# Performance work log

Measured on AMD Instinct MI355X. Metric: run time of the kernel, lower is better.

The kernel has to match this reference:

```python
import jax, jax.numpy as jnp
import numpy as np

GRID = (32, 32)          # 448 // 14
IMG = (448, 448)
SIGMA = 4.0              # anomalib AnomalyMapGenerator default smoothing


def _l2norm(x, axis=-1, eps=1e-12):
    return x / jnp.clip(jnp.linalg.norm(x, axis=axis, keepdims=True), eps, None)


def _gaussian_blur(x, sigma=SIGMA):
    # kornia-style: kernel_size = 2*int(4*sigma+0.5)+1, reflect padding, separable conv
    radius = int(4.0 * sigma + 0.5)
    t = jnp.arange(-radius, radius + 1, dtype=x.dtype)
    k = jnp.exp(-0.5 * (t / sigma) ** 2)
    k = k / k.sum()
    xp = jnp.pad(x, ((0, 0), (0, 0), (radius, radius), (radius, radius)), mode='reflect')
    kh = k.reshape(1, 1, -1, 1)
    kw = k.reshape(1, 1, 1, -1)
    dn = ('NCHW', 'OIHW', 'NCHW')
    y = jax.lax.conv_general_dilated(xp, kh, (1, 1), 'VALID', dimension_numbers=dn)
    return jax.lax.conv_general_dilated(y, kw, (1, 1), 'VALID', dimension_numbers=dn)


def setup_inputs() -> dict:
    key = jax.random.key(0)
    k1, k2 = jax.random.split(key)
    features = jax.random.normal(k1, (8, 1024, 384), dtype=jnp.float32)
    memory_bank = jax.random.normal(k2, (65536, 384), dtype=jnp.float32)
    return {"features": features, "memory_bank": memory_bank}


def reference(features, memory_bank):
    # features: (B, N, D) patch tokens from DINOv2; memory_bank: (M, D)
    b, n, _ = features.shape
    f = _l2norm(features)                 # F.normalize(features, p=2, dim=1) on flattened patches
    mb = _l2norm(memory_bank)             # bank stores normalized embeddings
    sim = jnp.einsum('bnd,md->bnm', f, mb)            # (B, N, M) cosine similarity
    dists = jnp.clip(1.0 - sim, 0.0, 2.0)
    min_dists = dists.min(axis=2)                     # k = num_neighbours = 1 -> row min
    num_top = max(int(n * 0.01), 1)
    top_vals = jax.lax.top_k(min_dists, num_top)[0]
    pred_score = top_vals.mean(axis=1, keepdims=True) # (B, 1)
    amap = min_dists.reshape(b, 1, *GRID)
    amap = jax.image.resize(amap, (b, 1, *IMG), method='bilinear')
    anomaly_map = _gaussian_blur(amap)                # (B, 1, H, W)
    return pred_score, anomaly_map
```

## Files before the change

kernel.cpp:

```cpp
#include <hip/hip_runtime.h>
#include <hip/hip_bf16.h>

#define NROW_F 8192
#define NROW_B 65536
#define KDIM   384
#define BM 128
#define BN 128
#define NSUB 16
#define NGRP (NROW_B / (BN * NSUB))
#define NBM  (NROW_F / BM)
#define NWG  (NBM * NGRP)

#define LDSA 0
#define LDSB 49152
#define LDSS 73728
#define LDSR 49152
#define LDS_TOT 81920

typedef int   i32x4 __attribute__((ext_vector_type(4)));
typedef float f32x4 __attribute__((ext_vector_type(4)));

static __device__ __forceinline__ void stage16(const void* g, void* l) {
  __builtin_amdgcn_global_load_lds(
      (const __attribute__((address_space(1))) unsigned int*)g,
      (__attribute__((address_space(3))) unsigned int*)l, 16, 0, 0);
}

__global__ __launch_bounds__(256) void quantize_rows_kernel(
    const float* __restrict__ in, char* __restrict__ out8,
    float* __restrict__ scales, int nrows) {
  int row  = blockIdx.x * 4 + (threadIdx.x >> 6);
  int lane = threadIdx.x & 63;
  if (row >= nrows) return;
  const float* r = in + (size_t)row * KDIM;
  float v[6];
  float ss = 0.f, mx = 0.f;
#pragma unroll
  for (int i = 0; i < 6; ++i) {
    v[i] = r[lane + i * 64];
    ss += v[i] * v[i];
    mx = fmaxf(mx, fabsf(v[i]));
  }
#pragma unroll
  for (int d = 1; d < 64; d <<= 1) {
    ss += __shfl_xor(ss, d, 64);
    mx = fmaxf(mx, __shfl_xor(mx, d, 64));
  }
  mx = fmaxf(mx, 1e-30f);
  float inv = rsqrtf(fmaxf(ss, 1e-24f));
  float scl = 127.0f / mx;
  if (lane == 0) scales[row] = mx * inv * (1.0f / 127.0f);
  char* o = out8 + (size_t)row * KDIM;
#pragma unroll
  for (int i = 0; i < 6; ++i)
    o[lane + i * 64] = (char)__float2int_rn(v[i] * scl);
}

__global__ __launch_bounds__(256, 2) void maxsim_kernel(
    const char* __restrict__ F8,
    const char* __restrict__ B8,
    const float* __restrict__ sA,
    const float* __restrict__ sB,
    float* __restrict__ partial) {
  __shared__ __align__(16) char smem[LDS_TOT];

  const int tid  = threadIdx.x;
  const int wv   = tid >> 6;
  const int lane = tid & 63;
  const int l15  = lane & 15;
  const int lhi  = lane >> 4;
  const int wr   = wv >> 1;
  const int wc   = wv & 1;

  const int wg  = (blockIdx.x & 7) * (NWG / 8) + (blockIdx.x >> 3);
  const int bm  = wg & (NBM - 1);
  const int grp = wg >> 6;
  const size_t brow = (size_t)bm * BM;

  const int srow = tid >> 2;
  const int gsw  = (tid & 3) ^ ((tid >> 3) & 3);

  {
    const char* gA = F8 + (size_t)(brow + srow) * KDIM + gsw * 16;
    char* lA = smem + LDSA + wv * 1024;
#pragma unroll
    for (int kt = 0; kt < 6; ++kt) {
      stage16(gA + kt * 64,             lA + kt * 8192);
      stage16(gA + kt * 64 + 64 * KDIM, lA + kt * 8192 + 4096);
    }
  }
  {
    const char* gs = (const char*)(sB + (size_t)grp * 2048) + tid * 16;
    stage16(gs,        smem + LDSS + wv * 1024);
    stage16(gs + 4096, smem + LDSS + 4096 + wv * 1024);
  }

  auto stageB = [&](int s2, int koff, int buf) {
    const char* g = B8 + ((size_t)grp * 2048 + s2 * 128 + srow) * KDIM
                    + koff * 64 + gsw * 16;
    char* l = smem + LDSB + buf * 8192 + wv * 1024;
    stage16(g, l);
    stage16(g + (size_t)64 * KDIM, l + 4096);
  };
  stageB(0, 0, 0);
  stageB(0, 1, 1);
  stageB(0, 2, 2);

  const int cof = ((l15 >> 1) & 3) << 4;

  auto ldA8 = [&](int k6, int m) -> i32x4 {
    int byte = k6 * 8192 + (wr * 64 + m * 16 + l15) * 64 + ((lhi << 4) ^ cof);
    return *reinterpret_cast<const i32x4*>(smem + LDSA + byte);
  };
  auto ldB8 = [&](int buf, int n) -> i32x4 {
    int byte = buf * 8192 + (wc * 64 + n * 16 + l15) * 64 + ((lhi << 4) ^ cof);
    return *reinterpret_cast<const i32x4*>(smem + LDSB + byte);
  };

  i32x4 acc[4][4];
  f32x4 vm[4];
#pragma unroll
  for (int m = 0; m < 4; ++m) {
    vm[m] = f32x4{-1e30f, -1e30f, -1e30f, -1e30f};
#pragma unroll
    for (int n = 0; n < 4; ++n) acc[m][n] = i32x4{0, 0, 0, 0};
  }

  asm volatile("s_waitcnt vmcnt(4)" ::: "memory");
  __builtin_amdgcn_s_barrier();

  i32x4 a[6][4];
#pragma unroll
  for (int k6 = 0; k6 < 6; ++k6)
#pragma unroll
    for (int m = 0; m < 4; ++m) a[k6][m] = ldA8(k6, m);

  i32x4 bA[4], bB[4];
#pragma unroll
  for (int n = 0; n < 4; ++n) bA[n] = ldB8(0, n);
  asm volatile("s_waitcnt lgkmcnt(0)" ::: "memory");

#define PHASE(K6, BC, BN_) do {                                               \
    asm volatile("s_waitcnt vmcnt(2)" ::: "memory");   \
    __builtin_amdgcn_s_barrier();                      \
    __builtin_amdgcn_sched_barrier(0);                                        \
    _Pragma("unroll")                                                         \
    for (int n = 0; n < 4; ++n) BN_[n] = ldB8(((K6) + 1) % 3, n);             \
    {                                                                         \
      const int s2 = ((K6) < 3) ? sub : ((sub + 1) & (NSUB - 1));             \
      stageB(s2, ((K6) + 3) % 6, (K6) % 3);                                   \
    }                                                                         \
    __builtin_amdgcn_sched_barrier(0);                                        \
    __builtin_amdgcn_s_setprio(1);                                            \
    _Pragma("unroll")                                                         \
    for (int n = 0; n < 4; ++n)                                               \
      _Pragma("unroll")                                                       \
      for (int m = 0; m < 4; ++m)                                             \
        acc[m][n] = __builtin_amdgcn_mfma_i32_16x16x64_i8(                    \
            a[K6][m], BC[n], acc[m][n], 0, 0, 0);                             \
    __builtin_amdgcn_s_setprio(0);                                            \
    asm volatile("s_waitcnt lgkmcnt(0)" ::: "memory");                        \
    __builtin_amdgcn_sched_barrier(0);                                        \
  } while (0)

  for (int sub = 0; sub < NSUB; ++sub) {
    PHASE(0, bA, bB);
    PHASE(1, bB, bA);
    PHASE(2, bA, bB);
    PHASE(3, bB, bA);
    PHASE(4, bA, bB);
    PHASE(5, bB, bA);
    float sb[4];
#pragma unroll
    for (int n = 0; n < 4; ++n)
      sb[n] = *reinterpret_cast<const float*>(
          smem + LDSS + (sub * 128 + wc * 64 + n * 16 + l15) * 4);
#pragma unroll
    for (int m = 0; m < 4; ++m) {
#pragma unroll
      for (int n = 0; n < 4; ++n)
#pragma unroll
        for (int j = 0; j < 4; ++j)
          vm[m][j] = fmaxf(vm[m][j], (float)acc[m][n][j] * sb[n]);
#pragma unroll
      for (int n = 0; n < 4; ++n) acc[m][n] = i32x4{0, 0, 0, 0};
    }
  }
#undef PHASE

  asm volatile("s_waitcnt vmcnt(0)" ::: "memory");
#pragma unroll
  for (int d = 1; d < 16; d <<= 1)
#pragma unroll
    for (int m = 0; m < 4; ++m)
#pragma unroll
      for (int j = 0; j < 4; ++j)
        vm[m][j] = fmaxf(vm[m][j], __shfl_xor(vm[m][j], d, 64));

  float* red = (float*)(smem + LDSR);
  __syncthreads();
  if (l15 == 0) {
#pragma unroll
    for (int m = 0; m < 4; ++m)
#pragma unroll
      for (int j = 0; j < 4; ++j)
        red[wc * 128 + wr * 64 + m * 16 + lhi * 4 + j] = vm[m][j];
  }
  __syncthreads();
  if (tid < BM) {
    float x = fmaxf(red[tid], red[128 + tid]);
    partial[(size_t)grp * NROW_F + brow + tid] = x * sA[brow + tid];
  }
}

__global__ __launch_bounds__(256) void combine_kernel(
    const float* __restrict__ partial, float* __restrict__ md) {
  int r = blockIdx.x * 256 + threadIdx.x;
  if (r >= NROW_F) return;
  float m = -1e30f;
#pragma unroll
  for (int c = 0; c < NGRP; ++c) m = fmaxf(m, partial[(size_t)c * NROW_F + r]);
  float d = 1.0f - m;
  d = fminf(fmaxf(d, 0.0f), 2.0f);
  md[r] = d;
}

__global__ __launch_bounds__(256) void topk_kernel(
    const float* __restrict__ md, float* __restrict__ out) {
  __shared__ float buf[1024];
  __shared__ float svals[256];
  __shared__ int   sidx[256];
  int b = blockIdx.x, tid = threadIdx.x;
  for (int i = tid; i < 1024; i += 256) buf[i] = md[b * 1024 + i];
  __syncthreads();
  float total = 0.f;
  for (int it = 0; it < 10; ++it) {
    float best = -1e30f; int bi = 0;
    for (int i = tid; i < 1024; i += 256)
      if (buf[i] > best) { best = buf[i]; bi = i; }
    svals[tid] = best; sidx[tid] = bi;
    __syncthreads();
    for (int s = 128; s > 0; s >>= 1) {
      if (tid < s && svals[tid + s] > svals[tid]) {
        svals[tid] = svals[tid + s]; sidx[tid] = sidx[tid + s];
      }
      __syncthreads();
    }
    if (tid == 0) { total += svals[0]; buf[sidx[0]] = -1e30f; }
    __syncthreads();
  }
  if (tid == 0) out[b] = total * 0.1f;
}

__global__ __launch_bounds__(256) void build_w_kernel(float* __restrict__ W) {
  int idx = blockIdx.x * 256 + threadIdx.x;
  if (idx >= 448 * 32) return;
  int y = idx >> 5, g = idx & 31;
  float ksum = 0.f, acc = 0.f;
#pragma unroll
  for (int t = -16; t <= 16; ++t) {
    float ft = (float)t * 0.25f;
    float kv = expf(-0.5f * ft * ft);
    ksum += kv;
    int p = y + t;
    p = (p < 0) ? -p : ((p > 447) ? 894 - p : p);
    float src = ((float)p + 0.5f) * (1.0f / 14.0f) - 0.5f;
    float fl = floorf(src);
    int i0 = (int)fl;
    float fr = src - fl;
    int c0 = i0 < 0 ? 0 : (i0 > 31 ? 31 : i0);
    int i1 = i0 + 1;
    int c1 = i1 < 0 ? 0 : (i1 > 31 ? 31 : i1);
    float w = 0.f;
    if (c0 == g) w += 1.0f - fr;
    if (c1 == g) w += fr;
    acc += kv * w;
  }
  W[idx] = acc / ksum;
}

__global__ __launch_bounds__(256) void map_stage1_kernel(
    const float* __restrict__ md, const float* __restrict__ W,
    float* __restrict__ tmp) {
  int idx = blockIdx.x * 256 + threadIdx.x;
  if (idx >= 8 * 448 * 32) return;
  int gx = idx & 31;
  int y  = (idx >> 5) % 448;
  int b  = idx / (448 * 32);
  const float* w = W + y * 32;
  const float* m = md + b * 1024 + gx;
  float s = 0.f;
#pragma unroll
  for (int gy = 0; gy < 32; ++gy) s += w[gy] * m[gy * 32];
  tmp[idx] = s;
}

__global__ __launch_bounds__(256) void map_stage2_kernel(
    const float* __restrict__ tmp, const float* __restrict__ W,
    float* __restrict__ out) {
  int idx = blockIdx.x * 256 + threadIdx.x;
  if (idx >= 8 * 448 * 448) return;
  int x    = idx % 448;
  int ypos = idx / 448;
  const float* w = W + x * 32;
  const float* t = tmp + ypos * 32;
  float s = 0.f;
#pragma unroll
  for (int gx = 0; gx < 32; ++gx) s += w[gx] * t[gx];
  out[idx] = s;
}

extern "C" void kernel_launch(void* const* d_in, const int* in_sizes, int n_in,
                              void* d_out, int out_size, void* d_ws, size_t ws_size,
                              hipStream_t stream) {
  const float* features = (const float*)d_in[0];
  const float* bank     = (const float*)d_in[1];
  float* out = (float*)d_out;

  char* ws = (char*)d_ws;
  char*  mb8     = ws;
  char*  f8      = ws + 25165824;
  float* sB      = (float*)(ws + 28311552);
  float* sA      = (float*)(ws + 28573696);
  float* partial = (float*)(ws + 28606464);
  float* md      = (float*)(ws + 29655040);
  float* W       = (float*)(ws + 29687808);
  float* tmp     = (float*)(ws + 29745152);

  quantize_rows_kernel<<<NROW_B / 4, 256, 0, stream>>>(bank, mb8, sB, NROW_B);
  quantize_rows_kernel<<<NROW_F / 4, 256, 0, stream>>>(features, f8, sA, NROW_F);
  maxsim_kernel<<<NWG, 256, 0, stream>>>(f8, mb8, sA, sB, partial);
  combine_kernel<<<NROW_F / 256, 256, 0, stream>>>(partial, md);
  topk_kernel<<<8, 256, 0, stream>>>(md, out);
  build_w_kernel<<<(448 * 32 + 255) / 256, 256, 0, stream>>>(W);
  map_stage1_kernel<<<(8 * 448 * 32 + 255) / 256, 256, 0, stream>>>(md, W, tmp);
  map_stage2_kernel<<<(8 * 448 * 448 + 255) / 256, 256, 0, stream>>>(tmp, W, out + 8);
}
```

Measured before the change: 247.7 us.

## Vectorize quantization, fuse post-processing kernels, and use wave-level top-k

```diff
diff --git a/kernel.cpp b/kernel.cpp
--- a/kernel.cpp
+++ b/kernel.cpp
@@ -29,31 +29,40 @@
 __global__ __launch_bounds__(256) void quantize_rows_kernel(
     const float* __restrict__ in, char* __restrict__ out8,
     float* __restrict__ scales, int nrows) {
-  int row  = blockIdx.x * 4 + (threadIdx.x >> 6);
-  int lane = threadIdx.x & 63;
+  int row = blockIdx.x * 8 + (threadIdx.x >> 5);
+  int l   = threadIdx.x & 31;
   if (row >= nrows) return;
-  const float* r = in + (size_t)row * KDIM;
-  float v[6];
+  const f32x4* r = (const f32x4*)(in + (size_t)row * KDIM);
+  f32x4 v[3];
   float ss = 0.f, mx = 0.f;
 #pragma unroll
-  for (int i = 0; i < 6; ++i) {
-    v[i] = r[lane + i * 64];
-    ss += v[i] * v[i];
-    mx = fmaxf(mx, fabsf(v[i]));
-  }
-#pragma unroll
-  for (int d = 1; d < 64; d <<= 1) {
+  for (int i = 0; i < 3; ++i) {
+    v[i] = r[l + i * 32];
+#pragma unroll
+    for (int j = 0; j < 4; ++j) {
+      ss += v[i][j] * v[i][j];
+      mx = fmaxf(mx, fabsf(v[i][j]));
+    }
+  }
+#pragma unroll
+  for (int d = 1; d < 32; d <<= 1) {
     ss += __shfl_xor(ss, d, 64);
     mx = fmaxf(mx, __shfl_xor(mx, d, 64));
   }
   mx = fmaxf(mx, 1e-30f);
   float inv = rsqrtf(fmaxf(ss, 1e-24f));
   float scl = 127.0f / mx;
-  if (lane == 0) scales[row] = mx * inv * (1.0f / 127.0f);
+  if (l == 0) scales[row] = mx * inv * (1.0f / 127.0f);
   char* o = out8 + (size_t)row * KDIM;
 #pragma unroll
-  for (int i = 0; i < 6; ++i)
-    o[lane + i * 64] = (char)__float2int_rn(v[i] * scl);
+  for (int i = 0; i < 3; ++i) {
+    char4 c;
+    c.x = (char)__float2int_rn(v[i][0] * scl);
+    c.y = (char)__float2int_rn(v[i][1] * scl);
+    c.z = (char)__float2int_rn(v[i][2] * scl);
+    c.w = (char)__float2int_rn(v[i][3] * scl);
+    *(char4*)(o + (l + i * 32) * 4) = c;
+  }
 }
 
 __global__ __launch_bounds__(256, 2) void maxsim_kernel(
@@ -141,8 +150,8 @@
   asm volatile("s_waitcnt lgkmcnt(0)" ::: "memory");
 
 #define PHASE(K6, BC, BN_) do {                                               \
-    asm volatile("s_waitcnt vmcnt(2)" ::: "memory");   \
-    __builtin_amdgcn_s_barrier();                      \
+    asm volatile("s_waitcnt vmcnt(2)" ::: "memory");                          \
+    __builtin_amdgcn_s_barrier();                                             \
     __builtin_amdgcn_sched_barrier(0);                                        \
     _Pragma("unroll")                                                         \
     for (int n = 0; n < 4; ++n) BN_[n] = ldB8(((K6) + 1) % 3, n);             \
@@ -213,48 +222,19 @@
   }
 }
 
-__global__ __launch_bounds__(256) void combine_kernel(
-    const float* __restrict__ partial, float* __restrict__ md) {
-  int r = blockIdx.x * 256 + threadIdx.x;
-  if (r >= NROW_F) return;
-  float m = -1e30f;
-#pragma unroll
-  for (int c = 0; c < NGRP; ++c) m = fmaxf(m, partial[(size_t)c * NROW_F + r]);
-  float d = 1.0f - m;
-  d = fminf(fmaxf(d, 0.0f), 2.0f);
-  md[r] = d;
-}
-
-__global__ __launch_bounds__(256) void topk_kernel(
-    const float* __restrict__ md, float* __restrict__ out) {
-  __shared__ float buf[1024];
-  __shared__ float svals[256];
-  __shared__ int   sidx[256];
-  int b = blockIdx.x, tid = threadIdx.x;
-  for (int i = tid; i < 1024; i += 256) buf[i] = md[b * 1024 + i];
-  __syncthreads();
-  float total = 0.f;
-  for (int it = 0; it < 10; ++it) {
-    float best = -1e30f; int bi = 0;
-    for (int i = tid; i < 1024; i += 256)
-      if (buf[i] > best) { best = buf[i]; bi = i; }
-    svals[tid] = best; sidx[tid] = bi;
-    __syncthreads();
-    for (int s = 128; s > 0; s >>= 1) {
-      if (tid < s && svals[tid + s] > svals[tid]) {
-        svals[tid] = svals[tid + s]; sidx[tid] = sidx[tid + s];
-      }
-      __syncthreads();
-    }
-    if (tid == 0) { total += svals[0]; buf[sidx[0]] = -1e30f; }
-    __syncthreads();
-  }
-  if (tid == 0) out[b] = total * 0.1f;
-}
-
-__global__ __launch_bounds__(256) void build_w_kernel(float* __restrict__ W) {
-  int idx = blockIdx.x * 256 + threadIdx.x;
-  if (idx >= 448 * 32) return;
+__global__ __launch_bounds__(256) void combw_kernel(
+    const float* __restrict__ partial, float* __restrict__ md,
+    float* __restrict__ W) {
+  if (blockIdx.x < 32) {
+    int r = blockIdx.x * 256 + threadIdx.x;
+    float m = -1e30f;
+#pragma unroll
+    for (int c = 0; c < NGRP; ++c) m = fmaxf(m, partial[(size_t)c * NROW_F + r]);
+    float d = 1.0f - m;
+    md[r] = fminf(fmaxf(d, 0.0f), 2.0f);
+    return;
+  }
+  int idx = (blockIdx.x - 32) * 256 + threadIdx.x;
   int y = idx >> 5, g = idx & 31;
   float ksum = 0.f, acc = 0.f;
 #pragma unroll
@@ -279,35 +259,62 @@
   W[idx] = acc / ksum;
 }
 
-__global__ __launch_bounds__(256) void map_stage1_kernel(
+__global__ __launch_bounds__(64) void topk_kernel(
+    const float* __restrict__ partial, float* __restrict__ out) {
+  int b = blockIdx.x, lane = threadIdx.x;
+  float vals[16];
+#pragma unroll
+  for (int k = 0; k < 16; ++k) {
+    int r = b * 1024 + k * 64 + lane;
+    float m = -1e30f;
+#pragma unroll
+    for (int c = 0; c < NGRP; ++c) m = fmaxf(m, partial[(size_t)c * NROW_F + r]);
+    float d = 1.0f - m;
+    vals[k] = fminf(fmaxf(d, 0.0f), 2.0f);
+  }
+  float total = 0.f;
+  for (int it = 0; it < 10; ++it) {
+    float lb = vals[0]; int li = 0;
+#pragma unroll
+    for (int k = 1; k < 16; ++k)
+      if (vals[k] > lb) { lb = vals[k]; li = k; }
+    float wm = lb;
+#pragma unroll
+    for (int d = 1; d < 64; d <<= 1) wm = fmaxf(wm, __shfl_xor(wm, d, 64));
+    unsigned long long mask = __ballot(lb == wm);
+    int winner = (int)(__ffsll((unsigned long long)mask) - 1);
+    bool kill = (lane == winner);
+#pragma unroll
+    for (int k = 0; k < 16; ++k)
+      vals[k] = (kill && k == li) ? -1e30f : vals[k];
+    total += wm;
+  }
+  if (lane == 0) out[b] = total * 0.1f;
+}
+
+__global__ __launch_bounds__(256) void map_kernel(
     const float* __restrict__ md, const float* __restrict__ W,
-    float* __restrict__ tmp) {
-  int idx = blockIdx.x * 256 + threadIdx.x;
-  if (idx >= 8 * 448 * 32) return;
-  int gx = idx & 31;
-  int y  = (idx >> 5) % 448;
-  int b  = idx / (448 * 32);
-  const float* w = W + y * 32;
-  const float* m = md + b * 1024 + gx;
-  float s = 0.f;
-#pragma unroll
-  for (int gy = 0; gy < 32; ++gy) s += w[gy] * m[gy * 32];
-  tmp[idx] = s;
-}
-
-__global__ __launch_bounds__(256) void map_stage2_kernel(
-    const float* __restrict__ tmp, const float* __restrict__ W,
     float* __restrict__ out) {
-  int idx = blockIdx.x * 256 + threadIdx.x;
-  if (idx >= 8 * 448 * 448) return;
-  int x    = idx % 448;
-  int ypos = idx / 448;
-  const float* w = W + x * 32;
-  const float* t = tmp + ypos * 32;
-  float s = 0.f;
-#pragma unroll
-  for (int gx = 0; gx < 32; ++gx) s += w[gx] * t[gx];
-  out[idx] = s;
+  __shared__ float tmpv[32];
+  int y = blockIdx.x % 448;
+  int b = blockIdx.x / 448;
+  int tid = threadIdx.x;
+  if (tid < 32) {
+    const float* w = W + y * 32;
+    const float* m = md + b * 1024 + tid;
+    float s = 0.f;
+#pragma unroll
+    for (int gy = 0; gy < 32; ++gy) s += w[gy] * m[gy * 32];
+    tmpv[tid] = s;
+  }
+  __syncthreads();
+  for (int x = tid; x < 448; x += 256) {
+    const float* w = W + x * 32;
+    float s = 0.f;
+#pragma unroll
+    for (int gx = 0; gx < 32; ++gx) s += w[gx] * tmpv[gx];
+    out[(size_t)blockIdx.x * 448 + x] = s;
+  }
 }
 
 extern "C" void kernel_launch(void* const* d_in, const int* in_sizes, int n_in,
@@ -325,14 +332,11 @@
   float* partial = (float*)(ws + 28606464);
   float* md      = (float*)(ws + 29655040);
   float* W       = (float*)(ws + 29687808);
-  float* tmp     = (float*)(ws + 29745152);
-
-  quantize_rows_kernel<<<NROW_B / 4, 256, 0, stream>>>(bank, mb8, sB, NROW_B);
-  quantize_rows_kernel<<<NROW_F / 4, 256, 0, stream>>>(features, f8, sA, NROW_F);
+
+  quantize_rows_kernel<<<NROW_B / 8, 256, 0, stream>>>(bank, mb8, sB, NROW_B);
+  quantize_rows_kernel<<<NROW_F / 8, 256, 0, stream>>>(features, f8, sA, NROW_F);
   maxsim_kernel<<<NWG, 256, 0, stream>>>(f8, mb8, sA, sB, partial);
-  combine_kernel<<<NROW_F / 256, 256, 0, stream>>>(partial, md);
-  topk_kernel<<<8, 256, 0, stream>>>(md, out);
-  build_w_kernel<<<(448 * 32 + 255) / 256, 256, 0, stream>>>(W);
-  map_stage1_kernel<<<(8 * 448 * 32 + 255) / 256, 256, 0, stream>>>(md, W, tmp);
-  map_stage2_kernel<<<(8 * 448 * 448 + 255) / 256, 256, 0, stream>>>(tmp, W, out + 8);
-}
+  combw_kernel<<<88, 256, 0, stream>>>(partial, md, W);
+  topk_kernel<<<8, 64, 0, stream>>>(partial, out);
+  map_kernel<<<8 * 448, 256, 0, stream>>>(md, W, out + 8);
+}
```

After: 240.2 us. -3.0%, faster.
